# Optimization experiments

Measured on AMD Instinct MI355X. Metric: run time of the kernel, lower is better.

## Reference

```python
import jax, jax.numpy as jnp
import numpy as np

SH_C0 = 0.28209479177387814
SH_C1 = 0.4886025119029199
SH_C2 = (1.0925484305920792, -1.0925484305920792, 0.31539156525252005, -1.0925484305920792, 0.5462742152960396)
SH_C3 = (-0.5900435899266435, 2.890611442640554, -0.4570457994644658, 0.3731763325901154, -0.4570457994644658, 1.445305721320277, -0.5900435899266435)

BG = 128  # gaussians per compositing block


def quat_to_rot(q):
    # q: [N,4] normalized quaternion (w,x,y,z) -> [N,3,3]
    w, x, y, z = q[:, 0], q[:, 1], q[:, 2], q[:, 3]
    R = jnp.stack([
        1 - 2 * (y * y + z * z), 2 * (x * y - w * z), 2 * (x * z + w * y),
        2 * (x * y + w * z), 1 - 2 * (x * x + z * z), 2 * (y * z - w * x),
        2 * (x * z - w * y), 2 * (y * z + w * x), 1 - 2 * (x * x + y * y)],
        axis=-1)
    return R.reshape(-1, 3, 3)


def eval_sh(sh, d):
    # sh: [N,16,3] degree-3 SH coeffs; d: [N,3] unit view dirs -> [N,3] rgb
    x, y, z = d[:, 0:1], d[:, 1:2], d[:, 2:3]
    xx, yy, zz = x * x, y * y, z * z
    xy, yz, xz = x * y, y * z, x * z
    res = SH_C0 * sh[:, 0]
    res = res - SH_C1 * y * sh[:, 1] + SH_C1 * z * sh[:, 2] - SH_C1 * x * sh[:, 3]
    res = (res + SH_C2[0] * xy * sh[:, 4] + SH_C2[1] * yz * sh[:, 5]
           + SH_C2[2] * (2 * zz - xx - yy) * sh[:, 6]
           + SH_C2[3] * xz * sh[:, 7] + SH_C2[4] * (xx - yy) * sh[:, 8])
    res = (res + SH_C3[0] * y * (3 * xx - yy) * sh[:, 9] + SH_C3[1] * xy * z * sh[:, 10]
           + SH_C3[2] * y * (4 * zz - xx - yy) * sh[:, 11]
           + SH_C3[3] * z * (2 * zz - 3 * xx - 3 * yy) * sh[:, 12]
           + SH_C3[4] * x * (4 * zz - xx - yy) * sh[:, 13]
           + SH_C3[5] * z * (xx - yy) * sh[:, 14] + SH_C3[6] * x * (xx - 3 * yy) * sh[:, 15])
    return res


def gs_forward(pws, shs, alphas_raw, scales_raw, rots_raw, us, Rcw, tcw, intr, height, width):
    fx, fy, cx, cy = intr[0], intr[1], intr[2], intr[3]
    N = pws.shape[0]
    HW = height * width

    # activations (GSModel.forward)
    alphas = jax.nn.sigmoid(alphas_raw[:, 0])          # [N]
    scales = jnp.exp(scales_raw)                       # [N,3]
    rots = rots_raw / jnp.linalg.norm(rots_raw, axis=1, keepdims=True)

    # gsc.project
    pcs = pws @ Rcw.T + tcw                            # [N,3] camera frame
    depth = pcs[:, 2]
    zs = jnp.where(depth > 0.2, depth, 1.0)            # safe divide for culled pts
    u = jnp.stack([fx * pcs[:, 0] / zs + cx, fy * pcs[:, 1] / zs + cy], axis=-1)
    # the `us` input is a grad-capture dummy; forward value comes from projection
    u = u + us - jax.lax.stop_gradient(us)

    # gsc.computeCov3D: Cov3d = (R S)(R S)^T
    R = quat_to_rot(rots)
    M = R * scales[:, None, :]
    cov3d = M @ jnp.swapaxes(M, 1, 2)                  # [N,3,3]

    # gsc.computeCov2D: cov2d = J W Cov3d W^T J^T + 0.3 I
    tanfx = width / (2.0 * fx)
    tanfy = height / (2.0 * fy)
    tx = jnp.clip(pcs[:, 0] / zs, -1.3 * tanfx, 1.3 * tanfx) * zs
    ty = jnp.clip(pcs[:, 1] / zs, -1.3 * tanfy, 1.3 * tanfy) * zs
    zero = jnp.zeros_like(zs)
    J = jnp.stack([
        fx / zs, zero, -fx * tx / (zs * zs),
        zero, fy / zs, -fy * ty / (zs * zs)], axis=-1).reshape(N, 2, 3)
    T = jnp.einsum('nij,jk->nik', J, Rcw)              # [N,2,3]
    cov2d = jnp.einsum('nij,njk,nlk->nil', T, cov3d, T)
    cov2d = cov2d + 0.3 * jnp.eye(2, dtype=cov2d.dtype)
    a, b, c = cov2d[:, 0, 0], cov2d[:, 0, 1], cov2d[:, 1, 1]
    det = a * c - b * b
    valid = (depth > 0.2) & (det > 0)
    det_s = jnp.where(valid, det, 1.0)

    # gsc.inverseCov2D: conic + screen-space radius (areas)
    cinv = jnp.stack([c / det_s, -b / det_s, a / det_s], axis=-1)  # [N,3]
    mid = 0.5 * (a + c)
    lam = mid + jnp.sqrt(jnp.maximum(mid * mid - det, 0.1))
    radius = jnp.where(valid, jnp.ceil(3.0 * jnp.sqrt(lam)), 0.0)
    areas = jnp.stack([radius, radius], axis=-1)       # [N,2]

    # gsc.sh2Color
    twc = -Rcw.T @ tcw
    dirs = pws - twc
    dirs = dirs / jnp.linalg.norm(dirs, axis=1, keepdims=True)
    colors = jnp.maximum(eval_sh(shs.reshape(N, 16, 3), dirs) + 0.5, 0.0)  # [N,3]

    # gsc.splat: depth-sorted front-to-back alpha compositing over all pixels
    order = jnp.argsort(depth)
    nb = N // BG
    u_s = u[order].reshape(nb, BG, 2)
    cinv_s = cinv[order].reshape(nb, BG, 3)
    al_s = alphas[order].reshape(nb, BG)
    col_s = colors[order].reshape(nb, BG, 3)
    val_s = valid[order].reshape(nb, BG)

    ys, xs = jnp.meshgrid(jnp.arange(height, dtype=jnp.float32),
                          jnp.arange(width, dtype=jnp.float32), indexing='ij')
    px = xs.ravel()
    py = ys.ravel()

    @jax.checkpoint
    def body(carry, blk):
        logT, acc = carry                              # [HW], [3,HW]
        ub, cb, ab, colb, vb = blk
        dx = px[None, :] - ub[:, 0:1]                  # [BG,HW]
        dy = py[None, :] - ub[:, 1:2]
        power = -0.5 * (cb[:, 0:1] * dx * dx + cb[:, 2:3] * dy * dy) - cb[:, 1:2] * dx * dy
        alp = jnp.minimum(0.99, ab[:, None] * jnp.exp(power))
        alp = jnp.where((power <= 0) & (alp >= 1.0 / 255.0) & vb[:, None], alp, 0.0)
        l1m = jnp.log1p(-alp)
        cs = jnp.cumsum(l1m, axis=0)
        logT_i = logT[None, :] + jnp.concatenate(
            [jnp.zeros((1, HW), l1m.dtype), cs[:-1]], axis=0)  # exclusive transmittance
        Ti = jnp.exp(logT_i)
        w = jnp.where(Ti > 1e-4, alp * Ti, 0.0)        # early-termination at tau<1e-4
        acc = acc + jnp.einsum('gp,gc->cp', w, colb)
        return (logT + cs[-1], acc), None

    init = (jnp.zeros(HW, dtype=jnp.float32), jnp.zeros((3, HW), dtype=jnp.float32))
    (_, acc), _ = jax.lax.scan(body, init, (u_s, cinv_s, al_s, col_s, val_s))
    image = acc.reshape(3, height, width)
    return image, areas


def setup_inputs() -> dict:
    key = jax.random.key(0)
    ks = jax.random.split(key, 6)
    N, H, W = 8192, 256, 256
    pws = jax.random.normal(ks[0], (N, 3), jnp.float32) * 2.0 + jnp.array([0.0, 0.0, 6.0])
    shs = jax.random.normal(ks[1], (N, 48), jnp.float32) * 0.3
    alphas_raw = jax.random.normal(ks[2], (N, 1), jnp.float32)
    scales_raw = jax.random.normal(ks[3], (N, 3), jnp.float32) * 0.3 - 3.0
    rots_raw = jax.random.normal(ks[4], (N, 4), jnp.float32)
    us = jnp.zeros((N, 2), jnp.float32)
    Rcw = jnp.eye(3, dtype=jnp.float32)
    tcw = jnp.zeros((3,), jnp.float32)
    intr = jnp.array([400.0, 400.0, 128.0, 128.0], jnp.float32)  # fx, fy, cx, cy
    return {"pws": pws, "shs": shs, "alphas_raw": alphas_raw, "scales_raw": scales_raw,
            "rots_raw": rots_raw, "us": us, "Rcw": Rcw, "tcw": tcw, "intr": intr,
            "height": H, "width": W}


def reference(pws, shs, alphas_raw, scales_raw, rots_raw, us, Rcw, tcw, intr, height, width):
    return gs_forward(pws, shs, alphas_raw, scales_raw, rots_raw, us, Rcw, tcw, intr, height, width)
```

## Files before the change

kernel.cpp:

```cpp
#include <hip/hip_runtime.h>

__global__ __launch_bounds__(256) void k_pre(
    const float* __restrict__ pws, const float* __restrict__ shs,
    const float* __restrict__ alphas_raw, const float* __restrict__ scales_raw,
    const float* __restrict__ rots_raw, const float* __restrict__ Rcw,
    const float* __restrict__ tcw, const float* __restrict__ intr,
    int N, int W, int H, float* __restrict__ areas,
    unsigned long long* __restrict__ keys, unsigned* __restrict__ rank,
    float* __restrict__ P)
{
    int i = blockIdx.x * 256 + threadIdx.x;
    if (i >= N) return;
    rank[i] = 0u;

    float R00=Rcw[0],R01=Rcw[1],R02=Rcw[2];
    float R10=Rcw[3],R11=Rcw[4],R12=Rcw[5];
    float R20=Rcw[6],R21=Rcw[7],R22=Rcw[8];
    float t0=tcw[0],t1=tcw[1],t2=tcw[2];
    float fx=intr[0],fy=intr[1],cx=intr[2],cy=intr[3];

    float pwx=pws[i*3+0], pwy=pws[i*3+1], pwz=pws[i*3+2];
    float pcx = R00*pwx + R01*pwy + R02*pwz + t0;
    float pcy = R10*pwx + R11*pwy + R12*pwz + t1;
    float pcz = R20*pwx + R21*pwy + R22*pwz + t2;
    float depth = pcz;
    float zs = (depth > 0.2f) ? depth : 1.0f;
    float u0 = fx * pcx / zs + cx;
    float u1 = fy * pcy / zs + cy;

    float qw=rots_raw[i*4+0], qx=rots_raw[i*4+1], qy=rots_raw[i*4+2], qz=rots_raw[i*4+3];
    float qn = sqrtf(qw*qw + qx*qx + qy*qy + qz*qz);
    qw/=qn; qx/=qn; qy/=qn; qz/=qn;
    float s0 = expf(scales_raw[i*3+0]);
    float s1 = expf(scales_raw[i*3+1]);
    float s2 = expf(scales_raw[i*3+2]);

    float xx=qx*qx, yy=qy*qy, zq=qz*qz;
    float xy=qx*qy, xz=qx*qz, yz=qy*qz;
    float wx=qw*qx, wy=qw*qy, wz=qw*qz;
    float r00=1.f-2.f*(yy+zq), r01=2.f*(xy-wz),     r02=2.f*(xz+wy);
    float r10=2.f*(xy+wz),     r11=1.f-2.f*(xx+zq), r12=2.f*(yz-wx);
    float r20=2.f*(xz-wy),     r21=2.f*(yz+wx),     r22=1.f-2.f*(xx+yy);

    float m00=r00*s0, m01=r01*s1, m02=r02*s2;
    float m10=r10*s0, m11=r11*s1, m12=r12*s2;
    float m20=r20*s0, m21=r21*s1, m22=r22*s2;
    float V00=m00*m00+m01*m01+m02*m02;
    float V01=m00*m10+m01*m11+m02*m12;
    float V02=m00*m20+m01*m21+m02*m22;
    float V11=m10*m10+m11*m11+m12*m12;
    float V12=m10*m20+m11*m21+m12*m22;
    float V22=m20*m20+m21*m21+m22*m22;

    float tanfx = (float)W / (2.f*fx), tanfy = (float)H / (2.f*fy);
    float limx = 1.3f*tanfx, limy = 1.3f*tanfy;
    float txl = fminf(fmaxf(pcx/zs, -limx), limx) * zs;
    float tyl = fminf(fmaxf(pcy/zs, -limy), limy) * zs;
    float iz = 1.f/zs, iz2 = iz*iz;
    float J00 = fx*iz, J02 = -fx*txl*iz2;
    float J11 = fy*iz, J12 = -fy*tyl*iz2;

    float T00=J00*R00+J02*R20, T01=J00*R01+J02*R21, T02=J00*R02+J02*R22;
    float T10=J11*R10+J12*R20, T11=J11*R11+J12*R21, T12=J11*R12+J12*R22;
    float A0=T00*V00+T01*V01+T02*V02;
    float A1=T00*V01+T01*V11+T02*V12;
    float A2=T00*V02+T01*V12+T02*V22;
    float B0=T10*V00+T11*V01+T12*V02;
    float B1=T10*V01+T11*V11+T12*V12;
    float B2=T10*V02+T11*V12+T12*V22;
    float ca = A0*T00+A1*T01+A2*T02 + 0.3f;
    float cb = A0*T10+A1*T11+A2*T12;
    float cc = B0*T10+B1*T11+B2*T12 + 0.3f;

    float det = ca*cc - cb*cb;
    bool valid = (depth > 0.2f) && (det > 0.f);
    float det_s = valid ? det : 1.f;
    float dinv = 1.f/det_s;
    float ci0 =  cc*dinv, ci1 = -cb*dinv, ci2 = ca*dinv;
    float mid = 0.5f*(ca+cc);
    float lam = mid + sqrtf(fmaxf(mid*mid - det, 0.1f));
    float radius = valid ? ceilf(3.f*sqrtf(lam)) : 0.f;
    areas[2*i+0] = radius;
    areas[2*i+1] = radius;

    float alpha = 1.f/(1.f + expf(-alphas_raw[i]));

    float tw0 = -(R00*t0 + R10*t1 + R20*t2);
    float tw1 = -(R01*t0 + R11*t1 + R21*t2);
    float tw2 = -(R02*t0 + R12*t1 + R22*t2);
    float dx_=pwx-tw0, dy_=pwy-tw1, dz_=pwz-tw2;
    float dn = sqrtf(dx_*dx_+dy_*dy_+dz_*dz_);
    float x=dx_/dn, y=dy_/dn, z=dz_/dn;
    float sxx=x*x, syy=y*y, szz=z*z;
    float sxy=x*y, syz=y*z, sxz=x*z;
    const float* sh = shs + i*48;
    float col[3];
    #pragma unroll
    for (int c = 0; c < 3; ++c) {
        float res = 0.28209479177387814f*sh[0*3+c];
        res += -0.4886025119029199f*y*sh[1*3+c]
             +  0.4886025119029199f*z*sh[2*3+c]
             + -0.4886025119029199f*x*sh[3*3+c];
        res +=  1.0925484305920792f*sxy*sh[4*3+c]
             + -1.0925484305920792f*syz*sh[5*3+c]
             +  0.31539156525252005f*(2.f*szz-sxx-syy)*sh[6*3+c]
             + -1.0925484305920792f*sxz*sh[7*3+c]
             +  0.5462742152960396f*(sxx-syy)*sh[8*3+c];
        res += -0.5900435899266435f*y*(3.f*sxx-syy)*sh[9*3+c]
             +  2.890611442640554f*sxy*z*sh[10*3+c]
             + -0.4570457994644658f*y*(4.f*szz-sxx-syy)*sh[11*3+c]
             +  0.3731763325901154f*z*(2.f*szz-3.f*sxx-3.f*syy)*sh[12*3+c]
             + -0.4570457994644658f*x*(4.f*szz-sxx-syy)*sh[13*3+c]
             +  1.445305721320277f*z*(sxx-syy)*sh[14*3+c]
             + -0.5900435899266435f*x*(sxx-3.f*syy)*sh[15*3+c];
        col[c] = fmaxf(res + 0.5f, 0.f);
    }

    float rc2;
    if (!valid || 255.f*alpha < 0.999f) {
        rc2 = -1.f;
    } else {
        float r2 = 2.f*lam*logf(255.f*alpha);
        float r  = sqrtf(fmaxf(r2, 0.f)) + 1.f;
        rc2 = r*r;
    }

    P[0*N+i]=u0;  P[1*N+i]=u1;  P[2*N+i]=ci0; P[3*N+i]=ci1; P[4*N+i]=ci2;
    P[5*N+i]=alpha; P[6*N+i]=col[0]; P[7*N+i]=col[1]; P[8*N+i]=col[2];
    P[9*N+i]=rc2;

    unsigned ud = __float_as_uint(depth);
    ud = (ud & 0x80000000u) ? ~ud : (ud | 0x80000000u);
    keys[i] = ((unsigned long long)ud << 32) | (unsigned)i;
}

#define JC 512
__global__ __launch_bounds__(256) void k_rank(
    const unsigned long long* __restrict__ keys, int N,
    unsigned* __restrict__ rank)
{
    __shared__ unsigned long long sk[JC];
    const int j0 = blockIdx.y * JC;
    for (int t = threadIdx.x; t < JC; t += 256) {
        int j = j0 + t;
        sk[t] = (j < N) ? keys[j] : ~0ull;
    }
    __syncthreads();

    const int i0 = blockIdx.x * 512 + threadIdx.x;
    const int i1 = i0 + 256;
    unsigned long long my0 = (i0 < N) ? keys[i0] : 0ull;
    unsigned long long my1 = (i1 < N) ? keys[i1] : 0ull;

    int c0 = 0, c1 = 0;
    const ulonglong2* sk2 = (const ulonglong2*)sk;
    #pragma unroll 4
    for (int t = 0; t < JC/2; ++t) {
        ulonglong2 kk = sk2[t];
        c0 += (kk.x < my0) ? 1 : 0;
        c0 += (kk.y < my0) ? 1 : 0;
        c1 += (kk.x < my1) ? 1 : 0;
        c1 += (kk.y < my1) ? 1 : 0;
    }
    if (i0 < N) atomicAdd(&rank[i0], (unsigned)c0);
    if (i1 < N) atomicAdd(&rank[i1], (unsigned)c1);
}

__global__ __launch_bounds__(256) void k_scatter(
    const unsigned* __restrict__ rank, const float* __restrict__ Pun,
    float4* __restrict__ gA, float4* __restrict__ gB,
    float4* __restrict__ cull, int N)
{
    int i = blockIdx.x * 256 + threadIdx.x;
    if (i >= N) return;
    int s = (int)rank[i];
    cull[s] = make_float4(Pun[0*N+i], Pun[1*N+i], Pun[9*N+i], 0.f);
    gA[s]   = make_float4(Pun[2*N+i], Pun[3*N+i], Pun[4*N+i], Pun[5*N+i]);
    gB[s]   = make_float4(Pun[6*N+i], Pun[7*N+i], Pun[8*N+i], 0.f);
}

__global__ __launch_bounds__(256) void k_render(
    const float4* __restrict__ gA, const float4* __restrict__ gB,
    const float4* __restrict__ cull, int N, int W, int H,
    int nTiles, int nseg, float4* __restrict__ segbuf)
{
    const int tid = threadIdx.x;
    const int tilesX = (W + 15) >> 4;
    const int tile = blockIdx.x % nTiles, seg = blockIdx.x / nTiles;
    const int tX = tile % tilesX, tY = tile / tilesX;
    const int ix = (tX << 4) + (tid & 15);
    const int iy = (tY << 4) + (tid >> 4);
    const bool inb = (ix < W) && (iy < H);
    const float pxf = (float)ix, pyf = (float)iy;
    const float tx0 = (float)(tX << 4), ty0 = (float)(tY << 4);
    int tx1i = (tX << 4) + 15; if (tx1i > W-1) tx1i = W-1;
    int ty1i = (tY << 4) + 15; if (ty1i > H-1) ty1i = H-1;
    const float tx1 = (float)tx1i, ty1 = (float)ty1i;

    const int per = (N + nseg - 1) / nseg;
    const int g0 = seg * per;
    const int g1 = min(N, g0 + per);

    float T = inb ? 1.f : 0.f;
    float aR = 0.f, aG = 0.f, aB = 0.f;

    __shared__ float4 sG0[256];
    __shared__ float4 sG1[256];
    __shared__ float  sB2[256];
    __shared__ unsigned long long sMask[4];

    const int wave = tid >> 6, lane = tid & 63;

    for (int base = g0; base < g1; base += 256) {
        int g = base + tid;
        bool ov = false;
        float u0=0.f, u1=0.f;
        float4 a4 = make_float4(0.f,0.f,0.f,0.f);
        float4 b4 = make_float4(0.f,0.f,0.f,0.f);
        if (g < g1) {
            float4 cu = cull[g];
            u0 = cu.x; u1 = cu.y;
            float cxp = fminf(fmaxf(u0, tx0), tx1);
            float cyp = fminf(fmaxf(u1, ty0), ty1);
            float ddx = u0 - cxp, ddy = u1 - cyp;
            ov = (ddx*ddx + ddy*ddy) <= cu.z;
            if (ov) { a4 = gA[g]; b4 = gB[g]; }
        }
        unsigned long long m = __ballot(ov);
        if (lane == 0) sMask[wave] = m;
        __syncthreads();
        int cnt = 0, off = 0;
        #pragma unroll
        for (int w2 = 0; w2 < 4; ++w2) {
            int pc = __popcll(sMask[w2]);
            if (w2 < wave) off += pc;
            cnt += pc;
        }
        if (ov) {
            int pos = off + __popcll(m & ((1ull << lane) - 1ull));
            sG0[pos] = make_float4(u0, u1, a4.x, a4.y);
            sG1[pos] = make_float4(a4.z, a4.w, b4.x, b4.y);
            sB2[pos] = b4.z;
        }
        __syncthreads();

        for (int e = 0; e < cnt; ++e) {
            float4 e0 = sG0[e];
            float4 e1 = sG1[e];
            float  gb = sB2[e];
            float ddx = pxf - e0.x, ddy = pyf - e0.y;
            float power = -0.5f*(e0.z*ddx*ddx + e1.x*ddy*ddy) - e0.w*ddx*ddy;
            float alp = fminf(0.99f, e1.y * __expf(power));
            alp = (power <= 0.f && alp >= (1.0f/255.0f)) ? alp : 0.f;
            float w = (T > 0.0001f) ? alp * T : 0.f;
            aR = fmaf(w, e1.z, aR);
            aG = fmaf(w, e1.w, aG);
            aB = fmaf(w, gb, aB);
            T = T - T * alp;
        }
        int done = (T <= 0.0001f) ? 1 : 0;
        if (__syncthreads_and(done)) break;
    }

    if (inb) {
        int pix = iy * W + ix;
        segbuf[(size_t)seg * (size_t)(W*H) + pix] = make_float4(T, aR, aG, aB);
    }
}

__global__ __launch_bounds__(256) void k_combine(
    const float4* __restrict__ segbuf, int HW, int nseg,
    float* __restrict__ out)
{
    int p = blockIdx.x * 256 + threadIdx.x;
    if (p >= HW) return;
    float T = 1.f, r = 0.f, g = 0.f, b = 0.f;
    for (int s = 0; s < nseg; ++s) {
        float4 v = segbuf[(size_t)s * HW + p];
        r = fmaf(T, v.y, r);
        g = fmaf(T, v.z, g);
        b = fmaf(T, v.w, b);
        T *= v.x;
    }
    out[p] = r; out[HW + p] = g; out[2*HW + p] = b;
}

extern "C" void kernel_launch(void* const* d_in, const int* in_sizes, int n_in,
                              void* d_out, int out_size, void* d_ws, size_t ws_size,
                              hipStream_t stream) {
    const float* pws        = (const float*)d_in[0];
    const float* shs        = (const float*)d_in[1];
    const float* alphas_raw = (const float*)d_in[2];
    const float* scales_raw = (const float*)d_in[3];
    const float* rots_raw   = (const float*)d_in[4];
    const float* Rcw        = (const float*)d_in[6];
    const float* tcw        = (const float*)d_in[7];
    const float* intr       = (const float*)d_in[8];

    const int N  = in_sizes[0] / 3;
    const int HW = (out_size - 2 * N) / 3;
    int W = 1; while ((long long)W * W < (long long)HW) ++W;
    const int H = HW / W;

    float* out   = (float*)d_out;
    float* areas = out + 3 * HW;

    char* ws = (char*)d_ws;
    size_t off = 0;
    unsigned long long* keys = (unsigned long long*)(ws + off); off += (size_t)N * 8;
    unsigned* rank = (unsigned*)(ws + off);                     off += (size_t)N * 4;
    off = (off + 15) & ~(size_t)15;
    float* Pun = (float*)(ws + off);                            off += (size_t)10 * N * 4;
    off = (off + 15) & ~(size_t)15;
    float4* cullv = (float4*)(ws + off);                        off += (size_t)N * 16;
    float4* gA = (float4*)(ws + off);                           off += (size_t)N * 16;
    float4* gB = (float4*)(ws + off);                           off += (size_t)N * 16;
    float4* segbuf = (float4*)(ws + off);
    size_t remain = (ws_size > off) ? (ws_size - off) : 0;
    int nseg = 4;
    while (nseg > 1 && (size_t)nseg * (size_t)HW * 16 > remain) nseg >>= 1;

    int gsN = (N + 255) / 256;
    k_pre<<<gsN, 256, 0, stream>>>(pws, shs, alphas_raw, scales_raw, rots_raw,
                                   Rcw, tcw, intr, N, W, H, areas, keys, rank, Pun);
    dim3 rgrid((N + 511) / 512, (N + JC - 1) / JC);
    k_rank<<<rgrid, 256, 0, stream>>>(keys, N, rank);
    k_scatter<<<gsN, 256, 0, stream>>>(rank, Pun, gA, gB, cullv, N);
    int tilesX = (W + 15) / 16, tilesY = (H + 15) / 16;
    int nTiles = tilesX * tilesY;
    k_render<<<nTiles * nseg, 256, 0, stream>>>(gA, gB, cullv, N, W, H,
                                                nTiles, nseg, segbuf);
    k_combine<<<(HW + 255) / 256, 256, 0, stream>>>(segbuf, HW, nseg, out);
}
```

Measured before the change: 109.2 us.

## Bin gaussians into per-tile bitmasks during scatter instead of per-block culling

The scatter kernel now works out which 16x16 tiles each sorted gaussian overlaps and sets a bit in a per-tile bitmask with atomicOr. The render kernel then walks the set bits of its tile's mask in depth order and reads gaussian data directly from global memory. This replaces the old scheme, where every tile block culled all N gaussians and compacted them through shared memory with ballots and barriers. The cost is an N-by-tiles bitmask that must be cleared each call, atomic traffic for large splats, and uncoalesced per-gaussian global loads with no shared-memory staging.

```diff
diff --git a/kernel.cpp b/kernel.cpp
--- a/kernel.cpp
+++ b/kernel.cpp
@@ -7,9 +7,12 @@
     const float* __restrict__ tcw, const float* __restrict__ intr,
     int N, int W, int H, float* __restrict__ areas,
     unsigned long long* __restrict__ keys, unsigned* __restrict__ rank,
-    float* __restrict__ P)
+    float* __restrict__ P,
+    unsigned long long* __restrict__ tilemask, int maskWords)
 {
     int i = blockIdx.x * 256 + threadIdx.x;
+    for (int w = i; w < maskWords; w += gridDim.x * 256)
+        tilemask[w] = 0ull;
     if (i >= N) return;
     rank[i] = 0u;
 
@@ -168,94 +171,86 @@
 
 __global__ __launch_bounds__(256) void k_scatter(
     const unsigned* __restrict__ rank, const float* __restrict__ Pun,
-    float4* __restrict__ gA, float4* __restrict__ gB,
-    float4* __restrict__ cull, int N)
+    float4* __restrict__ gA, float4* __restrict__ gB, float* __restrict__ gC,
+    unsigned long long* __restrict__ tilemask, int nwords,
+    int tilesX, int tilesY, int W, int H, int N)
 {
     int i = blockIdx.x * 256 + threadIdx.x;
     if (i >= N) return;
     int s = (int)rank[i];
-    cull[s] = make_float4(Pun[0*N+i], Pun[1*N+i], Pun[9*N+i], 0.f);
-    gA[s]   = make_float4(Pun[2*N+i], Pun[3*N+i], Pun[4*N+i], Pun[5*N+i]);
-    gB[s]   = make_float4(Pun[6*N+i], Pun[7*N+i], Pun[8*N+i], 0.f);
+    float u0 = Pun[0*N+i], u1 = Pun[1*N+i], rc2 = Pun[9*N+i];
+    gA[s] = make_float4(u0, u1, Pun[2*N+i], Pun[3*N+i]);
+    gB[s] = make_float4(Pun[4*N+i], Pun[5*N+i], Pun[6*N+i], Pun[7*N+i]);
+    gC[s] = Pun[8*N+i];
+    if (rc2 < 0.f) return;
+
+    float r = sqrtf(rc2);
+    float fx0 = fminf(fmaxf(floorf((u0 - r) * 0.0625f), 0.f), (float)(tilesX-1));
+    float fx1 = fminf(fmaxf(floorf((u0 + r) * 0.0625f), 0.f), (float)(tilesX-1));
+    float fy0 = fminf(fmaxf(floorf((u1 - r) * 0.0625f), 0.f), (float)(tilesY-1));
+    float fy1 = fminf(fmaxf(floorf((u1 + r) * 0.0625f), 0.f), (float)(tilesY-1));
+    int tx0 = (int)fx0, tx1 = (int)fx1, ty0 = (int)fy0, ty1 = (int)fy1;
+
+    const int word = s >> 6;
+    const unsigned long long bit = 1ull << (s & 63);
+    for (int ty = ty0; ty <= ty1; ++ty) {
+        float by0 = (float)(ty << 4);
+        float by1 = (float)min((ty << 4) + 15, H - 1);
+        float cyp = fminf(fmaxf(u1, by0), by1);
+        float ddy = u1 - cyp;
+        for (int tx = tx0; tx <= tx1; ++tx) {
+            float bx0 = (float)(tx << 4);
+            float bx1 = (float)min((tx << 4) + 15, W - 1);
+            float cxp = fminf(fmaxf(u0, bx0), bx1);
+            float ddx = u0 - cxp;
+            if (ddx*ddx + ddy*ddy <= rc2) {
+                int tile = ty * tilesX + tx;
+                atomicOr(&tilemask[(size_t)tile * nwords + word], bit);
+            }
+        }
+    }
 }
 
 __global__ __launch_bounds__(256) void k_render(
     const float4* __restrict__ gA, const float4* __restrict__ gB,
-    const float4* __restrict__ cull, int N, int W, int H,
-    int nTiles, int nseg, float4* __restrict__ segbuf)
+    const float* __restrict__ gC,
+    const unsigned long long* __restrict__ tilemask, int nwords,
+    int W, int H, int nTiles, int nseg, float4* __restrict__ segbuf)
 {
     const int tid = threadIdx.x;
+    const int tile = blockIdx.x % nTiles, seg = blockIdx.x / nTiles;
     const int tilesX = (W + 15) >> 4;
-    const int tile = blockIdx.x % nTiles, seg = blockIdx.x / nTiles;
     const int tX = tile % tilesX, tY = tile / tilesX;
     const int ix = (tX << 4) + (tid & 15);
     const int iy = (tY << 4) + (tid >> 4);
     const bool inb = (ix < W) && (iy < H);
     const float pxf = (float)ix, pyf = (float)iy;
-    const float tx0 = (float)(tX << 4), ty0 = (float)(tY << 4);
-    int tx1i = (tX << 4) + 15; if (tx1i > W-1) tx1i = W-1;
-    int ty1i = (tY << 4) + 15; if (ty1i > H-1) ty1i = H-1;
-    const float tx1 = (float)tx1i, ty1 = (float)ty1i;
-
-    const int per = (N + nseg - 1) / nseg;
-    const int g0 = seg * per;
-    const int g1 = min(N, g0 + per);
 
     float T = inb ? 1.f : 0.f;
     float aR = 0.f, aG = 0.f, aB = 0.f;
 
-    __shared__ float4 sG0[256];
-    __shared__ float4 sG1[256];
-    __shared__ float  sB2[256];
-    __shared__ unsigned long long sMask[4];
-
-    const int wave = tid >> 6, lane = tid & 63;
-
-    for (int base = g0; base < g1; base += 256) {
-        int g = base + tid;
-        bool ov = false;
-        float u0=0.f, u1=0.f;
-        float4 a4 = make_float4(0.f,0.f,0.f,0.f);
-        float4 b4 = make_float4(0.f,0.f,0.f,0.f);
-        if (g < g1) {
-            float4 cu = cull[g];
-            u0 = cu.x; u1 = cu.y;
-            float cxp = fminf(fmaxf(u0, tx0), tx1);
-            float cyp = fminf(fmaxf(u1, ty0), ty1);
-            float ddx = u0 - cxp, ddy = u1 - cyp;
-            ov = (ddx*ddx + ddy*ddy) <= cu.z;
-            if (ov) { a4 = gA[g]; b4 = gB[g]; }
-        }
-        unsigned long long m = __ballot(ov);
-        if (lane == 0) sMask[wave] = m;
-        __syncthreads();
-        int cnt = 0, off = 0;
-        #pragma unroll
-        for (int w2 = 0; w2 < 4; ++w2) {
-            int pc = __popcll(sMask[w2]);
-            if (w2 < wave) off += pc;
-            cnt += pc;
-        }
-        if (ov) {
-            int pos = off + __popcll(m & ((1ull << lane) - 1ull));
-            sG0[pos] = make_float4(u0, u1, a4.x, a4.y);
-            sG1[pos] = make_float4(a4.z, a4.w, b4.x, b4.y);
-            sB2[pos] = b4.z;
-        }
-        __syncthreads();
-
-        for (int e = 0; e < cnt; ++e) {
-            float4 e0 = sG0[e];
-            float4 e1 = sG1[e];
-            float  gb = sB2[e];
-            float ddx = pxf - e0.x, ddy = pyf - e0.y;
-            float power = -0.5f*(e0.z*ddx*ddx + e1.x*ddy*ddy) - e0.w*ddx*ddy;
-            float alp = fminf(0.99f, e1.y * __expf(power));
+    const unsigned long long* mask = tilemask + (size_t)tile * nwords;
+    const int wps = (nwords + nseg - 1) / nseg;
+    const int w0 = seg * wps;
+    const int w1 = min(nwords, w0 + wps);
+
+    for (int w = w0; w < w1; ++w) {
+        unsigned long long bits = mask[w];
+        while (bits) {
+            int b = __builtin_ctzll(bits);
+            bits &= bits - 1ull;
+            int s = (w << 6) + b;
+            float4 q0 = gA[s];
+            float4 q1 = gB[s];
+            float  cb2 = gC[s];
+            float ddx = pxf - q0.x, ddy = pyf - q0.y;
+            float power = -0.5f*(q0.z*ddx*ddx + q1.x*ddy*ddy) - q0.w*ddx*ddy;
+            float alp = fminf(0.99f, q1.y * __expf(power));
             alp = (power <= 0.f && alp >= (1.0f/255.0f)) ? alp : 0.f;
-            float w = (T > 0.0001f) ? alp * T : 0.f;
-            aR = fmaf(w, e1.z, aR);
-            aG = fmaf(w, e1.w, aG);
-            aB = fmaf(w, gb, aB);
+            float wgt = (T > 0.0001f) ? alp * T : 0.f;
+            aR = fmaf(wgt, q1.z, aR);
+            aG = fmaf(wgt, q1.w, aG);
+            aB = fmaf(wgt, cb2, aB);
             T = T - T * alp;
         }
         int done = (T <= 0.0001f) ? 1 : 0;
@@ -305,6 +300,10 @@
     float* out   = (float*)d_out;
     float* areas = out + 3 * HW;
 
+    const int tilesX = (W + 15) / 16, tilesY = (H + 15) / 16;
+    const int nTiles = tilesX * tilesY;
+    const int nwords = (N + 63) / 64;
+
     char* ws = (char*)d_ws;
     size_t off = 0;
     unsigned long long* keys = (unsigned long long*)(ws + off); off += (size_t)N * 8;
@@ -312,9 +311,13 @@
     off = (off + 15) & ~(size_t)15;
     float* Pun = (float*)(ws + off);                            off += (size_t)10 * N * 4;
     off = (off + 15) & ~(size_t)15;
-    float4* cullv = (float4*)(ws + off);                        off += (size_t)N * 16;
     float4* gA = (float4*)(ws + off);                           off += (size_t)N * 16;
     float4* gB = (float4*)(ws + off);                           off += (size_t)N * 16;
+    float* gC  = (float*)(ws + off);                            off += (size_t)N * 4;
+    off = (off + 15) & ~(size_t)15;
+    unsigned long long* tilemask = (unsigned long long*)(ws + off);
+    off += (size_t)nTiles * nwords * 8;
+    off = (off + 15) & ~(size_t)15;
     float4* segbuf = (float4*)(ws + off);
     size_t remain = (ws_size > off) ? (ws_size - off) : 0;
     int nseg = 4;
@@ -322,13 +325,13 @@
 
     int gsN = (N + 255) / 256;
     k_pre<<<gsN, 256, 0, stream>>>(pws, shs, alphas_raw, scales_raw, rots_raw,
-                                   Rcw, tcw, intr, N, W, H, areas, keys, rank, Pun);
+                                   Rcw, tcw, intr, N, W, H, areas, keys, rank,
+                                   Pun, tilemask, nTiles * nwords);
     dim3 rgrid((N + 511) / 512, (N + JC - 1) / JC);
     k_rank<<<rgrid, 256, 0, stream>>>(keys, N, rank);
-    k_scatter<<<gsN, 256, 0, stream>>>(rank, Pun, gA, gB, cullv, N);
-    int tilesX = (W + 15) / 16, tilesY = (H + 15) / 16;
-    int nTiles = tilesX * tilesY;
-    k_render<<<nTiles * nseg, 256, 0, stream>>>(gA, gB, cullv, N, W, H,
-                                                nTiles, nseg, segbuf);
+    k_scatter<<<gsN, 256, 0, stream>>>(rank, Pun, gA, gB, gC, tilemask, nwords,
+                                       tilesX, tilesY, W, H, N);
+    k_render<<<nTiles * nseg, 256, 0, stream>>>(gA, gB, gC, tilemask, nwords,
+                                                W, H, nTiles, nseg, segbuf);
     k_combine<<<(HW + 255) / 256, 256, 0, stream>>>(segbuf, HW, nseg, out);
 }
```

Measured after the change: 138.6 us. 1.27x slower.
